# Kernel optimization log

Measured on AMD Instinct MI355X. Metric: run time of the kernel, lower is better.

The kernel has to match this reference:

```python
import jax, jax.numpy as jnp
import numpy as np
import math

B, T, F_ = 4, 1024, 1024
TO_DIM, FROM_DIM, LATENT, H = 1024, 1024, 1024, 16
HEAD_DIM = LATENT // H

def _linear_params(key, in_dim, out_dim):
    kw, kb = jax.random.split(key)
    bound = 1.0 / math.sqrt(in_dim)
    W = jax.random.uniform(kw, (out_dim, in_dim), minval=-bound, maxval=bound, dtype=jnp.float32)
    b = jax.random.uniform(kb, (out_dim,), minval=-bound, maxval=bound, dtype=jnp.float32)
    return W, b

def setup_inputs() -> dict:
    key = jax.random.key(0)
    ks = jax.random.split(key, 7)
    X_to = jax.random.normal(ks[0], (B, T, TO_DIM), dtype=jnp.float32)
    X_from = jax.random.normal(ks[1], (B, F_, FROM_DIM), dtype=jnp.float32)
    mask_from = jax.random.randint(ks[2], (B, T, F_), 0, 2, dtype=jnp.int32)
    Wq, bq = _linear_params(ks[3], TO_DIM, LATENT)
    Wk, bk = _linear_params(ks[4], FROM_DIM, LATENT)
    Wv, bv = _linear_params(ks[5], FROM_DIM, LATENT)
    Wo, bo = _linear_params(ks[6], LATENT, TO_DIM)
    return {"X_to": X_to, "X_from": X_from, "mask_from": mask_from,
            "Wq": Wq, "bq": bq, "Wk": Wk, "bk": bk, "Wv": Wv, "bv": bv, "Wo": Wo, "bo": bo}

def _split_heads(x):
    # [b, t, (h k)] -> [b, h, t, k]
    b, t, _ = x.shape
    return x.reshape(b, t, H, HEAD_DIM).transpose(0, 2, 1, 3)

def reference(X_to, X_from, mask_from, Wq, bq, Wk, bk, Wv, bv, Wo, bo):
    Q = _split_heads(X_to @ Wq.T + bq)
    # NOTE: source swaps names — K comes from v_linear, V from k_linear. Reproduced literally.
    K = _split_heads(X_from @ Wv.T + bv)
    V = _split_heads(X_from @ Wk.T + bk)
    attn = jnp.einsum('bhtk,bhfk->bhtf', Q, K) / math.sqrt(HEAD_DIM)
    attn = jnp.where(mask_from[:, None, :, :] == 0, jnp.float32(-10000.0), attn)
    attn = jax.nn.softmax(attn, axis=-1)
    out = jnp.einsum('bhtf,bhfk->bhtk', attn, V)  # [b,h,t,k]
    out = out.transpose(0, 2, 1, 3).reshape(X_to.shape[0], X_to.shape[1], LATENT)
    return out @ Wo.T + bo
```

## Files before the change

kernel.cpp:

```cpp
#include <hip/hip_runtime.h>
#include <hip/hip_bf16.h>
#include <math.h>

#define BB 4
#define TT 1024
#define FF 1024
#define DIM 1024
#define NH 16
#define HD 64
#define MROWS (BB * TT)
#define FB (FF / 64)

typedef __attribute__((ext_vector_type(8))) short short8;
typedef __attribute__((ext_vector_type(4))) float f32x4;
typedef __hip_bfloat16 bf16;

__device__ __forceinline__ void async_copy16(const void* g, void* l) {
    __builtin_amdgcn_global_load_lds((const __attribute__((address_space(1))) void*)g,
                                     (__attribute__((address_space(3))) void*)l,
                                     16, 0, 0);
}

struct ConvArgs {
    const float* src[6];
    bf16* dst[6];
    int nvec[6];
    int blk_end[6];
    const int* mask;
    unsigned long long* Mb;
};

__global__ __launch_bounds__(256) void convert_pack(ConvArgs a) {
    int bx = blockIdx.x;
    if (bx >= a.blk_end[5]) {
        const int lane = threadIdx.x & 63;
        const int waveId = (bx - a.blk_end[5]) * 4 + (threadIdx.x >> 6);
#pragma unroll
        for (int it = 0; it < 16; ++it) {
            int c = waveId * 16 + it;
            int v = a.mask[(size_t)c * 64 + lane];
            unsigned long long bits = __ballot(v != 0);
            if (lane == 0) a.Mb[c] = bits;
        }
        return;
    }
    int seg = 0;
#pragma unroll
    for (int k = 0; k < 5; ++k) if (bx >= a.blk_end[k]) seg = k + 1;
    int b0 = seg ? a.blk_end[seg - 1] : 0;
    int idx = (bx - b0) * 256 + threadIdx.x;
    if (idx >= a.nvec[seg]) return;
    float4 v = ((const float4*)a.src[seg])[idx];
    union { bf16 t[4]; ushort4 u; } o;
    o.t[0] = __float2bfloat16(v.x);
    o.t[1] = __float2bfloat16(v.y);
    o.t[2] = __float2bfloat16(v.z);
    o.t[3] = __float2bfloat16(v.w);
    *(ushort4*)(a.dst[seg] + 4 * (size_t)idx) = o.u;
}

#define BK 64

struct QkvArgs {
    const bf16* A[3]; const bf16* W[3]; const float* bias[3]; bf16* C[3];
    int N[3]; int biasRow[3];
};

__global__ __launch_bounds__(256) void gemm_qkv(QkvArgs q) {
    __shared__ bf16 smem[128 * 132];
    bf16* As = smem;
    bf16* Bs = smem + 128 * BK;

    const int op = blockIdx.z;
    const bf16* A = q.A[op];
    const bf16* W = q.W[op];
    const float* bias = q.bias[op];
    bf16* C = q.C[op];
    const int N = q.N[op];
    const int brow = q.biasRow[op];

    const int lin = blockIdx.x + 8 * blockIdx.y;
    const int xcd = lin & 7;
    const int t   = lin >> 3;
    int m0, n0;
    if (brow) {
        m0 = (((t & 7) + xcd) & 7) * 128;
        n0 = (xcd * 4 + (t >> 3)) * 128;
    } else {
        m0 = (xcd * 4 + (t >> 3)) * 128;
        n0 = (((t & 7) + xcd) & 7) * 128;
    }

    const int tid  = threadIdx.x;
    const int lane = tid & 63;
    const int wave = tid >> 6;
    const int quad = lane >> 4;
    const int l16  = lane & 15;
    const int wm = wave & 1;
    const int wn = wave >> 1;
    const int wbase = tid & ~63;

    f32x4 acc[4][4] = {};

    for (int k0 = 0; k0 < DIM; k0 += BK) {
#pragma unroll
        for (int j = 0; j < 4; ++j) {
            int slot = j * 256 + tid;
            int r = slot >> 3;
            int g = (slot & 7) ^ (r & 7);
            async_copy16(A + (size_t)(m0 + r) * DIM + k0 + g * 8,
                         As + (size_t)(j * 256 + wbase) * 8);
            async_copy16(W + (size_t)(n0 + r) * DIM + k0 + g * 8,
                         Bs + (size_t)(j * 256 + wbase) * 8);
        }
        __syncthreads();

#pragma unroll
        for (int kk = 0; kk < 2; ++kk) {
            short8 a[4], b[4];
#pragma unroll
            for (int mi = 0; mi < 4; ++mi) {
                int r = wm * 64 + mi * 16 + l16;
                int p = (kk * 4 + quad) ^ (r & 7);
                a[mi] = *(const short8*)(As + r * BK + p * 8);
            }
#pragma unroll
            for (int ni = 0; ni < 4; ++ni) {
                int r = wn * 64 + ni * 16 + l16;
                int p = (kk * 4 + quad) ^ (r & 7);
                b[ni] = *(const short8*)(Bs + r * BK + p * 8);
            }
#pragma unroll
            for (int mi = 0; mi < 4; ++mi)
#pragma unroll
                for (int ni = 0; ni < 4; ++ni)
                    acc[mi][ni] = __builtin_amdgcn_mfma_f32_16x16x32_bf16(
                        a[mi], b[ni], acc[mi][ni], 0, 0, 0);
        }
        __syncthreads();
    }

    bf16* Cs = smem;
#pragma unroll
    for (int ni = 0; ni < 4; ++ni) {
        const int nl = wn * 64 + ni * 16 + l16;
        float bcol = brow ? 0.0f : bias[n0 + nl];
#pragma unroll
        for (int mi = 0; mi < 4; ++mi)
#pragma unroll
            for (int i = 0; i < 4; ++i) {
                const int ml = wm * 64 + mi * 16 + quad * 4 + i;
                float v = acc[mi][ni][i] + (brow ? bias[m0 + ml] : bcol);
                Cs[ml * 132 + nl] = __float2bfloat16(v);
            }
    }
    __syncthreads();
#pragma unroll
    for (int j = 0; j < 8; ++j) {
        int slot = j * 256 + tid;
        int rr = slot >> 4, cc = slot & 15;
        short8 v = *(const short8*)(Cs + rr * 132 + cc * 8);
        *(short8*)(C + (size_t)(m0 + rr) * N + n0 + cc * 8) = v;
    }
}

__global__ __launch_bounds__(256) void gemm_o(
    const bf16* __restrict__ A, const bf16* __restrict__ W,
    const float* __restrict__ bias, float* __restrict__ C)
{
    __shared__ float smemf[128 * 66];
    bf16* As = (bf16*)smemf;
    bf16* Bs = As + 128 * BK;

    const int lin = blockIdx.x + 16 * blockIdx.y;
    const int xcd = lin & 7;
    const int t   = lin >> 3;
    const int m0 = (xcd * 4 + (t >> 4)) * 128;
    const int n0 = (((t & 15) + 2 * xcd) & 15) * 64;

    const int tid  = threadIdx.x;
    const int lane = tid & 63;
    const int wave = tid >> 6;
    const int quad = lane >> 4;
    const int l16  = lane & 15;
    const int wm = wave & 1;
    const int wn = wave >> 1;
    const int wbase = tid & ~63;

    f32x4 acc[4][2] = {};

    for (int k0 = 0; k0 < DIM; k0 += BK) {
#pragma unroll
        for (int j = 0; j < 4; ++j) {
            int slot = j * 256 + tid;
            int r = slot >> 3;
            int g = (slot & 7) ^ (r & 7);
            async_copy16(A + (size_t)(m0 + r) * DIM + k0 + g * 8,
                         As + (size_t)(j * 256 + wbase) * 8);
        }
#pragma unroll
        for (int j = 0; j < 2; ++j) {
            int slot = j * 256 + tid;
            int r = slot >> 3;
            int g = (slot & 7) ^ (r & 7);
            async_copy16(W + (size_t)(n0 + r) * DIM + k0 + g * 8,
                         Bs + (size_t)(j * 256 + wbase) * 8);
        }
        __syncthreads();

#pragma unroll
        for (int kk = 0; kk < 2; ++kk) {
            short8 a[4], b[2];
#pragma unroll
            for (int mi = 0; mi < 4; ++mi) {
                int r = wm * 64 + mi * 16 + l16;
                int p = (kk * 4 + quad) ^ (r & 7);
                a[mi] = *(const short8*)(As + r * BK + p * 8);
            }
#pragma unroll
            for (int ni = 0; ni < 2; ++ni) {
                int r = wn * 32 + ni * 16 + l16;
                int p = (kk * 4 + quad) ^ (r & 7);
                b[ni] = *(const short8*)(Bs + r * BK + p * 8);
            }
#pragma unroll
            for (int mi = 0; mi < 4; ++mi)
#pragma unroll
                for (int ni = 0; ni < 2; ++ni)
                    acc[mi][ni] = __builtin_amdgcn_mfma_f32_16x16x32_bf16(
                        a[mi], b[ni], acc[mi][ni], 0, 0, 0);
        }
        __syncthreads();
    }

    float* Cs = smemf;
#pragma unroll
    for (int ni = 0; ni < 2; ++ni) {
        const int nl = wn * 32 + ni * 16 + l16;
        const float bcol = bias[n0 + nl];
#pragma unroll
        for (int mi = 0; mi < 4; ++mi)
#pragma unroll
            for (int i = 0; i < 4; ++i) {
                const int ml = wm * 64 + mi * 16 + quad * 4 + i;
                Cs[ml * 66 + nl] = acc[mi][ni][i] + bcol;
            }
    }
    __syncthreads();
#pragma unroll
    for (int j = 0; j < 8; ++j) {
        int slot = j * 256 + tid;
        int rr = slot >> 4, cc = slot & 15;
        float4 v = *(const float4*)(Cs + rr * 66 + cc * 4);
        *(float4*)(C + (size_t)(m0 + rr) * DIM + n0 + cc * 4) = v;
    }
}

__global__ __launch_bounds__(256) void attn_kernel(
    const bf16* Qg, const bf16* __restrict__ Kg, const bf16* __restrict__ Vtg,
    const unsigned long long* __restrict__ Mbits, bf16* Og)
{
    __shared__ bf16 Ks[128 * 64];
    __shared__ bf16 Vts[64 * 128];
    __shared__ bf16 Ps[64 * 136];

    const int tid  = threadIdx.x;
    const int lane = tid & 63;
    const int wave = tid >> 6;
    const int quad = lane >> 4;
    const int l16  = lane & 15;

    const int lin = blockIdx.x + 16 * (blockIdx.y + 16 * blockIdx.z);
    const int xcd = lin & 7;
    const int t   = lin >> 3;
    const int bh  = xcd * 8 + (t >> 4);
    const int b   = bh >> 4;
    const int h   = bh & 15;
    const int t0  = (t & 15) * 64;

    const size_t qrow0 = (size_t)b * TT + t0;
    const size_t krow0 = (size_t)b * FF;
    const int wbase = tid & ~63;

    const bf16* qptr = Qg + (qrow0 + wave * 16 + l16) * DIM + h * HD;
    short8 qa0 = *(const short8*)(qptr + quad * 8);
    short8 qa1 = *(const short8*)(qptr + 32 + quad * 8);

    float lrow[4] = {0.f, 0.f, 0.f, 0.f};
    f32x4 oacc[4] = {};

    for (int f0 = 0; f0 < FF; f0 += 128) {
#pragma unroll
        for (int j = 0; j < 4; ++j) {
            int slot = j * 256 + tid;
            int rk = slot >> 3;
            int gk = (slot & 7) ^ (rk & 7);
            async_copy16(Kg + (krow0 + f0 + rk) * DIM + h * HD + gk * 8,
                         Ks + (size_t)(j * 256 + wbase) * 8);
            int rv = slot >> 4;
            int gv = (slot & 15) ^ (rv & 15);
            async_copy16(Vtg + (size_t)(h * HD + rv) * MROWS + b * FF + f0 + gv * 8,
                         Vts + (size_t)(j * 256 + wbase) * 8);
        }
        __syncthreads();

        f32x4 sacc[8] = {};
#pragma unroll
        for (int nt = 0; nt < 8; ++nt) {
            int r = nt * 16 + l16;
            short8 kb0 = *(const short8*)(Ks + r * 64 + ((quad       ^ (r & 7)) * 8));
            short8 kb1 = *(const short8*)(Ks + r * 64 + (((quad + 4) ^ (r & 7)) * 8));
            sacc[nt] = __builtin_amdgcn_mfma_f32_16x16x32_bf16(qa0, kb0, sacc[nt], 0, 0, 0);
            sacc[nt] = __builtin_amdgcn_mfma_f32_16x16x32_bf16(qa1, kb1, sacc[nt], 0, 0, 0);
        }

#pragma unroll
        for (int i = 0; i < 4; ++i) {
            const int prow = wave * 16 + quad * 4 + i;
#pragma unroll
            for (int half = 0; half < 2; ++half) {
                unsigned long long m64 = Mbits[(qrow0 + prow) * FB + (f0 >> 6) + half];
                unsigned long long sh = m64 >> l16;
                unsigned lo = (unsigned)sh, hi = (unsigned)(sh >> 32);
                const int sb = half * 4;
                float p0 = (lo & 1u)         ? __expf(sacc[sb + 0][i] * 0.125f) : 0.f;
                float p1 = ((lo >> 16) & 1u) ? __expf(sacc[sb + 1][i] * 0.125f) : 0.f;
                float p2 = (hi & 1u)         ? __expf(sacc[sb + 2][i] * 0.125f) : 0.f;
                float p3 = ((hi >> 16) & 1u) ? __expf(sacc[sb + 3][i] * 0.125f) : 0.f;
                lrow[i] += p0 + p1 + p2 + p3;
                Ps[prow * 136 + half * 64 +  0 + l16] = __float2bfloat16(p0);
                Ps[prow * 136 + half * 64 + 16 + l16] = __float2bfloat16(p1);
                Ps[prow * 136 + half * 64 + 32 + l16] = __float2bfloat16(p2);
                Ps[prow * 136 + half * 64 + 48 + l16] = __float2bfloat16(p3);
            }
        }

        short8 pa[4];
#pragma unroll
        for (int kf = 0; kf < 4; ++kf)
            pa[kf] = *(const short8*)(Ps + (wave * 16 + l16) * 136 + kf * 32 + quad * 8);
#pragma unroll
        for (int nt = 0; nt < 4; ++nt) {
            int rd = nt * 16 + l16;
#pragma unroll
            for (int kf = 0; kf < 4; ++kf) {
                int g = (kf * 4 + quad) ^ (rd & 15);
                short8 vb = *(const short8*)(Vts + rd * 128 + g * 8);
                oacc[nt] = __builtin_amdgcn_mfma_f32_16x16x32_bf16(pa[kf], vb, oacc[nt], 0, 0, 0);
            }
        }
        __syncthreads();
    }

#pragma unroll
    for (int i = 0; i < 4; ++i) {
        float l = lrow[i];
        l += __shfl_xor(l, 1);
        l += __shfl_xor(l, 2);
        l += __shfl_xor(l, 4);
        l += __shfl_xor(l, 8);
        float inv = 1.0f / l;
        const int prow = wave * 16 + quad * 4 + i;
#pragma unroll
        for (int nt = 0; nt < 4; ++nt)
            Ps[prow * 136 + nt * 16 + l16] = __float2bfloat16(oacc[nt][i] * inv);
    }
    __syncthreads();
#pragma unroll
    for (int j = 0; j < 2; ++j) {
        int s = j * 256 + tid;
        int rr = s >> 3, off = (s & 7) * 8;
        short8 v = *(const short8*)(Ps + rr * 136 + off);
        *(short8*)(Og + (qrow0 + rr) * DIM + h * HD + off) = v;
    }
}

extern "C" void kernel_launch(void* const* d_in, const int* in_sizes, int n_in,
                              void* d_out, int out_size, void* d_ws, size_t ws_size,
                              hipStream_t stream) {
    const float* X_to   = (const float*)d_in[0];
    const float* X_from = (const float*)d_in[1];
    const int*   mask   = (const int*)  d_in[2];
    const float* Wq     = (const float*)d_in[3];
    const float* bq     = (const float*)d_in[4];
    const float* Wk     = (const float*)d_in[5];
    const float* bk     = (const float*)d_in[6];
    const float* Wv     = (const float*)d_in[7];
    const float* bv     = (const float*)d_in[8];
    const float* Wo     = (const float*)d_in[9];
    const float* bo     = (const float*)d_in[10];
    float* out = (float*)d_out;

    char* ws = (char*)d_ws;
    bf16* Xt16 = (bf16*)(ws);
    bf16* Xf16 = (bf16*)(ws + (8u  << 20));
    bf16* Wq16 = (bf16*)(ws + (16u << 20));
    bf16* Wv16 = (bf16*)(ws + (18u << 20));
    bf16* Wk16 = (bf16*)(ws + (20u << 20));
    bf16* Wo16 = (bf16*)(ws + (22u << 20));
    bf16* Q16  = (bf16*)(ws + (24u << 20));
    bf16* K16  = (bf16*)(ws + (32u << 20));
    bf16* Vt16 = (bf16*)(ws + (40u << 20));
    unsigned long long* Mb = (unsigned long long*)(ws + (48u << 20));

    ConvArgs ca;
    ca.src[0] = X_to;   ca.dst[0] = Xt16; ca.nvec[0] = MROWS * DIM / 4;
    ca.src[1] = X_from; ca.dst[1] = Xf16; ca.nvec[1] = MROWS * DIM / 4;
    ca.src[2] = Wq;     ca.dst[2] = Wq16; ca.nvec[2] = DIM * DIM / 4;
    ca.src[3] = Wv;     ca.dst[3] = Wv16; ca.nvec[3] = DIM * DIM / 4;
    ca.src[4] = Wk;     ca.dst[4] = Wk16; ca.nvec[4] = DIM * DIM / 4;
    ca.src[5] = Wo;     ca.dst[5] = Wo16; ca.nvec[5] = DIM * DIM / 4;
    int cum = 0;
    for (int k = 0; k < 6; ++k) { cum += ca.nvec[k] / 256; ca.blk_end[k] = cum; }
    ca.mask = mask; ca.Mb = Mb;
    convert_pack<<<cum + 1024, 256, 0, stream>>>(ca);

    QkvArgs qa;
    qa.A[0] = Xt16; qa.W[0] = Wq16; qa.bias[0] = bq; qa.C[0] = Q16;
    qa.N[0] = DIM; qa.biasRow[0] = 0;
    qa.A[1] = Xf16; qa.W[1] = Wv16; qa.bias[1] = bv; qa.C[1] = K16;
    qa.N[1] = DIM; qa.biasRow[1] = 0;
    qa.A[2] = Wk16; qa.W[2] = Xf16; qa.bias[2] = bk; qa.C[2] = Vt16;
    qa.N[2] = MROWS; qa.biasRow[2] = 1;
    gemm_qkv<<<dim3(8, 32, 3), 256, 0, stream>>>(qa);

    attn_kernel<<<dim3(TT / 64, NH, BB), 256, 0, stream>>>(
        Q16, K16, Vt16, Mb, Q16);

    gemm_o<<<dim3(DIM / 64, MROWS / 128), 256, 0, stream>>>(Q16, Wo16, bo, out);
}
```

Measured before the change: 240.2 us.

## Transpose score MFMA so lanes pack P stores and preload mask words

New measurement: 230.0 us. 1.04x faster.

```diff
diff --git a/kernel.cpp b/kernel.cpp
--- a/kernel.cpp
+++ b/kernel.cpp
@@ -12,6 +12,7 @@
 #define FB (FF / 64)
 
 typedef __attribute__((ext_vector_type(8))) short short8;
+typedef __attribute__((ext_vector_type(4))) short short4v;
 typedef __attribute__((ext_vector_type(4))) float f32x4;
 typedef __hip_bfloat16 bf16;
 
@@ -256,13 +257,14 @@
     }
 }
 
-__global__ __launch_bounds__(256) void attn_kernel(
+__global__ __launch_bounds__(256, 4) void attn_kernel(
     const bf16* Qg, const bf16* __restrict__ Kg, const bf16* __restrict__ Vtg,
     const unsigned long long* __restrict__ Mbits, bf16* Og)
 {
     __shared__ bf16 Ks[128 * 64];
     __shared__ bf16 Vts[64 * 128];
-    __shared__ bf16 Ps[64 * 136];
+    __shared__ bf16 Pt[64 * 136];
+    __shared__ float ls[64];
 
     const int tid  = threadIdx.x;
     const int lane = tid & 63;
@@ -283,13 +285,20 @@
     const int wbase = tid & ~63;
 
     const bf16* qptr = Qg + (qrow0 + wave * 16 + l16) * DIM + h * HD;
-    short8 qa0 = *(const short8*)(qptr + quad * 8);
-    short8 qa1 = *(const short8*)(qptr + 32 + quad * 8);
-
-    float lrow[4] = {0.f, 0.f, 0.f, 0.f};
+    short8 qb0 = *(const short8*)(qptr + quad * 8);
+    short8 qb1 = *(const short8*)(qptr + 32 + quad * 8);
+
+    const unsigned long long* mrow = Mbits + (qrow0 + wave * 16 + l16) * FB;
+    unsigned long long mw[16];
+#pragma unroll
+    for (int w = 0; w < 16; ++w) mw[w] = mrow[w];
+
+    float lsum = 0.f;
     f32x4 oacc[4] = {};
 
-    for (int f0 = 0; f0 < FF; f0 += 128) {
+#pragma unroll
+    for (int it = 0; it < 8; ++it) {
+        const int f0 = it * 128;
 #pragma unroll
         for (int j = 0; j < 4; ++j) {
             int slot = j * 256 + tid;
@@ -304,41 +313,42 @@
         }
         __syncthreads();
 
-        f32x4 sacc[8] = {};
-#pragma unroll
-        for (int nt = 0; nt < 8; ++nt) {
-            int r = nt * 16 + l16;
-            short8 kb0 = *(const short8*)(Ks + r * 64 + ((quad       ^ (r & 7)) * 8));
-            short8 kb1 = *(const short8*)(Ks + r * 64 + (((quad + 4) ^ (r & 7)) * 8));
-            sacc[nt] = __builtin_amdgcn_mfma_f32_16x16x32_bf16(qa0, kb0, sacc[nt], 0, 0, 0);
-            sacc[nt] = __builtin_amdgcn_mfma_f32_16x16x32_bf16(qa1, kb1, sacc[nt], 0, 0, 0);
-        }
-
-#pragma unroll
-        for (int i = 0; i < 4; ++i) {
-            const int prow = wave * 16 + quad * 4 + i;
-#pragma unroll
-            for (int half = 0; half < 2; ++half) {
-                unsigned long long m64 = Mbits[(qrow0 + prow) * FB + (f0 >> 6) + half];
-                unsigned long long sh = m64 >> l16;
-                unsigned lo = (unsigned)sh, hi = (unsigned)(sh >> 32);
-                const int sb = half * 4;
-                float p0 = (lo & 1u)         ? __expf(sacc[sb + 0][i] * 0.125f) : 0.f;
-                float p1 = ((lo >> 16) & 1u) ? __expf(sacc[sb + 1][i] * 0.125f) : 0.f;
-                float p2 = (hi & 1u)         ? __expf(sacc[sb + 2][i] * 0.125f) : 0.f;
-                float p3 = ((hi >> 16) & 1u) ? __expf(sacc[sb + 3][i] * 0.125f) : 0.f;
-                lrow[i] += p0 + p1 + p2 + p3;
-                Ps[prow * 136 + half * 64 +  0 + l16] = __float2bfloat16(p0);
-                Ps[prow * 136 + half * 64 + 16 + l16] = __float2bfloat16(p1);
-                Ps[prow * 136 + half * 64 + 32 + l16] = __float2bfloat16(p2);
-                Ps[prow * 136 + half * 64 + 48 + l16] = __float2bfloat16(p3);
-            }
+        f32x4 sacc[8];
+#pragma unroll
+        for (int ft = 0; ft < 8; ++ft) {
+            int r = ft * 16 + l16;
+            short8 ka0 = *(const short8*)(Ks + r * 64 + ((quad       ^ (r & 7)) * 8));
+            short8 ka1 = *(const short8*)(Ks + r * 64 + (((quad + 4) ^ (r & 7)) * 8));
+            f32x4 s = {};
+            s = __builtin_amdgcn_mfma_f32_16x16x32_bf16(ka0, qb0, s, 0, 0, 0);
+            s = __builtin_amdgcn_mfma_f32_16x16x32_bf16(ka1, qb1, s, 0, 0, 0);
+            sacc[ft] = s;
+        }
+
+        const unsigned long long w0 = mw[2 * it];
+        const unsigned long long w1 = mw[2 * it + 1];
+#pragma unroll
+        for (int ft = 0; ft < 8; ++ft) {
+            const unsigned long long word = (ft < 4) ? w0 : w1;
+            const unsigned bits4 =
+                (unsigned)(word >> ((ft & 3) * 16 + quad * 4)) & 0xFu;
+            union { short4v v; short s[4]; } pk;
+            float psum = 0.f;
+#pragma unroll
+            for (int i = 0; i < 4; ++i) {
+                float p = (bits4 >> i) & 1u ? __expf(sacc[ft][i] * 0.125f) : 0.f;
+                psum += p;
+                pk.s[i] = (short)__bfloat16_as_ushort(__float2bfloat16(p));
+            }
+            lsum += psum;
+            *(short4v*)(Pt + l16 * 136 + wave * 0 + (wave * 16 + l16) * 0 +
+                        (wave * 16 + l16) * 136 - l16 * 136 + ft * 16 + quad * 4) = pk.v;
         }
 
         short8 pa[4];
 #pragma unroll
         for (int kf = 0; kf < 4; ++kf)
-            pa[kf] = *(const short8*)(Ps + (wave * 16 + l16) * 136 + kf * 32 + quad * 8);
+            pa[kf] = *(const short8*)(Pt + (wave * 16 + l16) * 136 + kf * 32 + quad * 8);
 #pragma unroll
         for (int nt = 0; nt < 4; ++nt) {
             int rd = nt * 16 + l16;
@@ -352,25 +362,24 @@
         __syncthreads();
     }
 
+    lsum += __shfl_xor(lsum, 16);
+    lsum += __shfl_xor(lsum, 32);
+    if (quad == 0) ls[wave * 16 + l16] = lsum;
+
 #pragma unroll
     for (int i = 0; i < 4; ++i) {
-        float l = lrow[i];
-        l += __shfl_xor(l, 1);
-        l += __shfl_xor(l, 2);
-        l += __shfl_xor(l, 4);
-        l += __shfl_xor(l, 8);
-        float inv = 1.0f / l;
+        float inv = 1.0f / ls[wave * 16 + quad * 4 + i];
         const int prow = wave * 16 + quad * 4 + i;
 #pragma unroll
         for (int nt = 0; nt < 4; ++nt)
-            Ps[prow * 136 + nt * 16 + l16] = __float2bfloat16(oacc[nt][i] * inv);
+            Pt[prow * 136 + nt * 16 + l16] = __float2bfloat16(oacc[nt][i] * inv);
     }
     __syncthreads();
 #pragma unroll
     for (int j = 0; j < 2; ++j) {
         int s = j * 256 + tid;
         int rr = s >> 3, off = (s & 7) * 8;
-        short8 v = *(const short8*)(Ps + rr * 136 + off);
+        short8 v = *(const short8*)(Pt + rr * 136 + off);
         *(short8*)(Og + (qrow0 + rr) * DIM + h * HD + off) = v;
     }
 }
```
